# Optimization experiments

Measured on AMD Instinct MI355X. Metric: run time of the kernel, lower is better.

Reference implementation:

```python
import jax, jax.numpy as jnp
import numpy as np

B, S, D, H = 2, 2048, 1024, 16
DQ = D // H
EPS = 1e-5


def setup_inputs() -> dict:
    key = jax.random.key(0)
    ks = jax.random.split(key, 6)
    scale = 0.02
    return {
        "x": jax.random.normal(ks[0], (B, S, D), dtype=jnp.float32),
        "ln_g": jnp.ones((D,), dtype=jnp.float32),
        "ln_b": jnp.zeros((D,), dtype=jnp.float32),
        "Wq": jax.random.normal(ks[1], (D, D), dtype=jnp.float32) * scale,
        "bq": jnp.zeros((D,), dtype=jnp.float32),
        "Wk": jax.random.normal(ks[2], (D, D), dtype=jnp.float32) * scale,
        "bk": jnp.zeros((D,), dtype=jnp.float32),
        "Wv": jax.random.normal(ks[3], (D, D), dtype=jnp.float32) * scale,
        "bv": jnp.zeros((D,), dtype=jnp.float32),
        "Wo": jax.random.normal(ks[4], (D, D), dtype=jnp.float32) * scale,
        "bo": jnp.zeros((D,), dtype=jnp.float32),
    }


def reference(x, ln_g, ln_b, Wq, bq, Wk, bk, Wv, bv, Wo, bo):
    # pre-LayerNorm (torch default eps=1e-5, biased variance)
    mu = jnp.mean(x, axis=-1, keepdims=True)
    var = jnp.mean((x - mu) ** 2, axis=-1, keepdims=True)
    xn = (x - mu) * jax.lax.rsqrt(var + EPS) * ln_g + ln_b

    # QKV projections; weights stored [d_in, d_out]
    q = xn @ Wq + bq  # [B,S,D]
    k = xn @ Wk + bk
    v = xn @ Wv + bv

    # split heads -> [B,H,S,DQ]
    def heads(t):
        return t.reshape(B, S, H, DQ).transpose(0, 2, 1, 3)
    q, k, v = heads(q), heads(k), heads(v)

    scores = jnp.einsum("bhqd,bhkd->bhqk", q, k) / jnp.sqrt(jnp.float32(DQ))
    causal = jnp.tril(jnp.ones((S, S), dtype=bool))  # True = keep
    scores = jnp.where(causal, scores, -jnp.inf)
    probs = jax.nn.softmax(scores, axis=-1)
    attn = jnp.einsum("bhqk,bhkd->bhqd", probs, v)  # [B,H,S,DQ]

    # merge heads: [B,H,S,DQ] -> [B,S,H*DQ] (matches transpose/flatten/transpose)
    merged = attn.transpose(0, 2, 1, 3).reshape(B, S, D)
    out = merged @ Wo + bo
    return out + x
```

## Files before the change

### kernel.cpp

```cpp
#include <hip/hip_runtime.h>
#include <math.h>

#define BB 2
#define SS 2048
#define DD 1024
#define HH 16
#define DQK 64
#define NROWS (BB * SS)
#define NE ((size_t)BB * SS * DD)

using short8 = __attribute__((ext_vector_type(8))) short;
using f32x4  = __attribute__((ext_vector_type(4))) float;

__device__ __forceinline__ ushort f2bf(float f) {
  union { float f; unsigned u; } c; c.f = f;
  return (ushort)((c.u + 0x7fffu + ((c.u >> 16) & 1u)) >> 16);
}

__device__ __forceinline__ unsigned cvt_pk_bf16(float lo, float hi) {
  unsigned r;
  asm("v_cvt_pk_bf16_f32 %0, %1, %2" : "=v"(r) : "v"(lo), "v"(hi));
  return r;
}

__device__ __forceinline__ f32x4 mfma16(short8 a, short8 b, f32x4 c) {
  return __builtin_amdgcn_mfma_f32_16x16x32_bf16(a, b, c, 0, 0, 0);
}

__device__ __forceinline__ float fmax3(float a, float b, float c) {
  return fmaxf(fmaxf(a, b), c);
}

typedef __attribute__((address_space(1))) const unsigned gas_u32;
typedef __attribute__((address_space(3))) unsigned las_u32;
__device__ __forceinline__ void gload_lds16(const void* g, void* l) {
  __builtin_amdgcn_global_load_lds((gas_u32*)g, (las_u32*)l, 16, 0, 0);
}

__global__ __launch_bounds__(256) void prep(const float* __restrict__ x,
                                            const float* __restrict__ g,
                                            const float* __restrict__ bta,
                                            ushort* __restrict__ xn,
                                            const float* __restrict__ Wq,
                                            const float* __restrict__ Wk,
                                            const float* __restrict__ Wv,
                                            const float* __restrict__ Wo,
                                            ushort* __restrict__ wt) {
  const int t = threadIdx.x;
  if (blockIdx.x < NROWS / 4) {
    const int lane = t & 63, wid = t >> 6;
    const int row = blockIdx.x * 4 + wid;
    const float4* xr = (const float4*)(x + (size_t)row * DD);
    float4 v[4];
    float s = 0.f, ss = 0.f;
#pragma unroll
    for (int c = 0; c < 4; ++c) {
      v[c] = xr[c * 64 + lane];
      s  += (v[c].x + v[c].y) + (v[c].z + v[c].w);
      ss += (v[c].x * v[c].x + v[c].y * v[c].y) +
            (v[c].z * v[c].z + v[c].w * v[c].w);
    }
#pragma unroll
    for (int off = 32; off > 0; off >>= 1) {
      s  += __shfl_xor(s, off);
      ss += __shfl_xor(ss, off);
    }
    const float mu  = s * (1.0f / DD);
    const float var = ss * (1.0f / DD) - mu * mu;
    const float inv = rsqrtf(var + 1e-5f);
    ushort4* xo = (ushort4*)(xn + (size_t)row * DD);
#pragma unroll
    for (int c = 0; c < 4; ++c) {
      const float4 g4 = ((const float4*)g)[c * 64 + lane];
      const float4 b4 = ((const float4*)bta)[c * 64 + lane];
      ushort4 o;
      o.x = f2bf((v[c].x - mu) * inv * g4.x + b4.x);
      o.y = f2bf((v[c].y - mu) * inv * g4.y + b4.y);
      o.z = f2bf((v[c].z - mu) * inv * g4.z + b4.z);
      o.w = f2bf((v[c].w - mu) * inv * g4.w + b4.w);
      xo[c * 64 + lane] = o;
    }
  } else {
    __shared__ float tile[64][65];
    const int wb = blockIdx.x - NROWS / 4;
    const int z = wb >> 8;
    const int k0 = (wb & 15) * 64, n0 = ((wb >> 4) & 15) * 64;
    const float* W = (z == 0) ? Wq : (z == 1) ? Wk : (z == 2) ? Wv : Wo;
    ushort* dst = wt + (size_t)z * DD * DD;
    const int tr = t >> 4, tc = (t & 15) * 4;
#pragma unroll
    for (int rr = 0; rr < 64; rr += 16) {
      float4 v = *(const float4*)(W + (size_t)(k0 + rr + tr) * DD + n0 + tc);
      tile[rr + tr][tc + 0] = v.x;
      tile[rr + tr][tc + 1] = v.y;
      tile[rr + tr][tc + 2] = v.z;
      tile[rr + tr][tc + 3] = v.w;
    }
    __syncthreads();
#pragma unroll
    for (int rr = 0; rr < 64; rr += 16) {
      const int n = rr + tr;
      ushort4 o;
      o.x = f2bf(tile[tc + 0][n]);
      o.y = f2bf(tile[tc + 1][n]);
      o.z = f2bf(tile[tc + 2][n]);
      o.w = f2bf(tile[tc + 3][n]);
      *(ushort4*)(dst + (size_t)(n0 + n) * DD + k0 + tc) = o;
    }
  }
}

#define GEMM_CORE(Ag, Bg)                                                     \
  f32x4 acc[4][4];                                                            \
  _Pragma("unroll")                                                           \
  for (int m = 0; m < 4; ++m)                                                 \
    _Pragma("unroll")                                                         \
    for (int n = 0; n < 4; ++n) acc[m][n] = (f32x4){0.f, 0.f, 0.f, 0.f};     \
  const int cs = ((t & 3) * 16) ^ (((t >> 3) & 3) * 16);                      \
  const int fsw = ((r16 >> 1) & 3) * 16;                                      \
  {                                                                           \
    GSTAGE(Ag, Bg, 0, 0);                                                     \
    GSTAGE(Ag, Bg, 1, 32);                                                    \
    int cb = 0;                                                               \
    for (int k0 = 0; k0 < DD; k0 += 32) {                                     \
      __builtin_amdgcn_sched_barrier(0);                                      \
      if (k0 + 32 < DD) {                                                     \
        asm volatile("s_waitcnt vmcnt(4)" ::: "memory");                      \
      } else {                                                                \
        asm volatile("s_waitcnt vmcnt(0)" ::: "memory");                      \
      }                                                                       \
      __builtin_amdgcn_s_barrier();                                           \
      __builtin_amdgcn_sched_barrier(0);                                      \
      if (k0 + 64 < DD) {                                                     \
        int nb = cb + 2; if (nb >= 3) nb -= 3;                                \
        GSTAGE(Ag, Bg, nb, k0 + 64);                                          \
      }                                                                       \
      const char* Ac = (const char*)&As[cb][0][0];                            \
      const char* Bc = (const char*)&Bs[cb][0][0];                            \
      short8 af[4], bf[4];                                                    \
      _Pragma("unroll")                                                       \
      for (int m = 0; m < 4; ++m)                                             \
        af[m] = *(const short8*)(Ac + (wr * 64 + m * 16 + r16) * 64 +         \
                                 ((g * 16) ^ fsw));                           \
      _Pragma("unroll")                                                       \
      for (int n = 0; n < 4; ++n)                                             \
        bf[n] = *(const short8*)(Bc + (wc * 64 + n * 16 + r16) * 64 +         \
                                 ((g * 16) ^ fsw));                           \
      _Pragma("unroll")                                                       \
      for (int m = 0; m < 4; ++m)                                             \
        _Pragma("unroll")                                                     \
        for (int n = 0; n < 4; ++n) acc[m][n] = mfma16(af[m], bf[n], acc[m][n]); \
      cb = (cb + 1 == 3) ? 0 : cb + 1;                                        \
    }                                                                         \
  }

#define GSTAGE(Ag, Bg, buf, k0)                                               \
  {                                                                           \
    _Pragma("unroll")                                                         \
    for (int i = 0; i < 2; ++i) {                                             \
      gload_lds16(Ag + (size_t)(row0 + i * 64 + (t >> 2)) * (DD * 2) +        \
                      (k0) * 2 + cs,                                          \
                  (char*)&As[buf][0][0] + i * 4096 + t * 16);                 \
      gload_lds16(Bg + (size_t)(col0 + i * 64 + (t >> 2)) * (DD * 2) +        \
                      (k0) * 2 + cs,                                          \
                  (char*)&Bs[buf][0][0] + i * 4096 + t * 16);                 \
    }                                                                         \
  }

#define GEMM_CORE_O(Ag, Bg)                                                   \
  f32x4 acc[4][2];                                                            \
  _Pragma("unroll")                                                           \
  for (int m = 0; m < 4; ++m)                                                 \
    _Pragma("unroll")                                                         \
    for (int n = 0; n < 2; ++n) acc[m][n] = (f32x4){0.f, 0.f, 0.f, 0.f};     \
  const int cs = ((t & 3) * 16) ^ (((t >> 3) & 3) * 16);                      \
  const int fsw = ((r16 >> 1) & 3) * 16;                                      \
  {                                                                           \
    GSTAGE_O(Ag, Bg, 0, 0);                                                   \
    GSTAGE_O(Ag, Bg, 1, 32);                                                  \
    int cb = 0;                                                               \
    for (int k0 = 0; k0 < DD; k0 += 32) {                                     \
      __builtin_amdgcn_sched_barrier(0);                                      \
      if (k0 + 32 < DD) {                                                     \
        asm volatile("s_waitcnt vmcnt(3)" ::: "memory");                      \
      } else {                                                                \
        asm volatile("s_waitcnt vmcnt(0)" ::: "memory");                      \
      }                                                                       \
      __builtin_amdgcn_s_barrier();                                           \
      __builtin_amdgcn_sched_barrier(0);                                      \
      if (k0 + 64 < DD) {                                                     \
        int nb = cb + 2; if (nb >= 3) nb -= 3;                                \
        GSTAGE_O(Ag, Bg, nb, k0 + 64);                                        \
      }                                                                       \
      const char* Ac = (const char*)&As[cb][0][0];                            \
      const char* Bc = (const char*)&Bs[cb][0][0];                            \
      short8 af[4], bf[2];                                                    \
      _Pragma("unroll")                                                       \
      for (int m = 0; m < 4; ++m)                                             \
        af[m] = *(const short8*)(Ac + (wr * 64 + m * 16 + r16) * 64 +         \
                                 ((g * 16) ^ fsw));                           \
      _Pragma("unroll")                                                       \
      for (int n = 0; n < 2; ++n)                                             \
        bf[n] = *(const short8*)(Bc + (wc * 32 + n * 16 + r16) * 64 +         \
                                 ((g * 16) ^ fsw));                           \
      _Pragma("unroll")                                                       \
      for (int m = 0; m < 4; ++m)                                             \
        _Pragma("unroll")                                                     \
        for (int n = 0; n < 2; ++n) acc[m][n] = mfma16(af[m], bf[n], acc[m][n]); \
      cb = (cb + 1 == 3) ? 0 : cb + 1;                                        \
    }                                                                         \
  }

#define GSTAGE_O(Ag, Bg, buf, k0)                                             \
  {                                                                           \
    _Pragma("unroll")                                                         \
    for (int i = 0; i < 2; ++i)                                               \
      gload_lds16(Ag + (size_t)(row0 + i * 64 + (t >> 2)) * (DD * 2) +        \
                      (k0) * 2 + cs,                                          \
                  (char*)&As[buf][0][0] + i * 4096 + t * 16);                 \
    gload_lds16(Bg + (size_t)(col0 + (t >> 2)) * (DD * 2) + (k0) * 2 + cs,    \
                (char*)&Bs[buf][0][0] + t * 16);                              \
  }

__global__ __launch_bounds__(256, 3) void gemm_qkv(
    const ushort* __restrict__ A, const ushort* __restrict__ wt,
    const float* __restrict__ bq, const float* __restrict__ bk,
    const float* __restrict__ bv, ushort* __restrict__ qb,
    ushort* __restrict__ kb, ushort* __restrict__ vt) {
  __shared__ ushort As[3][128][32];
  __shared__ ushort Bs[3][128][32];
  const int t = threadIdx.x;
  const int lane = t & 63;
  const int w = t >> 6, wr = w >> 1, wc = w & 1;
  const int r16 = lane & 15, g = lane >> 4;
  const int row0 = blockIdx.x * 128;
  const int mat = blockIdx.y >> 3;
  const int col0 = (blockIdx.y & 7) * 128;
  const char* Ag = (const char*)A;
  const char* Bg = (const char*)(wt + (size_t)mat * DD * DD);
  const float* bias = (mat == 0) ? bq : (mat == 1) ? bk : bv;
  const float scl = (mat == 0) ? 0.125f * 1.44269504f : 1.0f;

  GEMM_CORE(Ag, Bg)

#pragma unroll
  for (int n = 0; n < 4; ++n) {
    const int c = col0 + wc * 64 + n * 16 + r16;
    const float bc = bias[c];
#pragma unroll
    for (int m = 0; m < 4; ++m) {
      const int rbase = row0 + wr * 64 + m * 16 + g * 4;
      if (mat < 2) {
        ushort* outb = (mat == 0) ? qb : kb;
#pragma unroll
        for (int e = 0; e < 4; ++e)
          outb[(size_t)(rbase + e) * DD + c] = f2bf((acc[m][n][e] + bc) * scl);
      } else {
        uint2 st;
        st.x = cvt_pk_bf16(acc[m][n][0] + bc, acc[m][n][1] + bc);
        st.y = cvt_pk_bf16(acc[m][n][2] + bc, acc[m][n][3] + bc);
        const size_t vrow = (size_t)((rbase >> 11) * HH + (c >> 6)) * DQK + (c & 63);
        *(uint2*)(vt + vrow * SS + (rbase & 2047)) = st;
      }
    }
  }
}

__global__ __launch_bounds__(256, 2) void gemm_o(
    const ushort* __restrict__ A, const ushort* __restrict__ Bt,
    const float* __restrict__ bias, const float* __restrict__ resid,
    float* __restrict__ outf) {
  __shared__ ushort As[3][128][32];
  __shared__ ushort Bs[3][64][32];
  const int t = threadIdx.x;
  const int lane = t & 63;
  const int w = t >> 6, wr = w >> 1, wc = w & 1;
  const int r16 = lane & 15, g = lane >> 4;
  const int row0 = blockIdx.x * 128;
  const int col0 = blockIdx.y * 64;
  const char* Ag = (const char*)A;
  const char* Bg = (const char*)Bt;

  GEMM_CORE_O(Ag, Bg)

#pragma unroll
  for (int n = 0; n < 2; ++n) {
    const int c = col0 + wc * 32 + n * 16 + r16;
    const float bc = bias[c];
#pragma unroll
    for (int m = 0; m < 4; ++m) {
      const int rbase = row0 + wr * 64 + m * 16 + g * 4;
#pragma unroll
      for (int e = 0; e < 4; ++e) {
        const size_t idx = (size_t)(rbase + e) * DD + c;
        outf[idx] = acc[m][n][e] + bc + resid[idx];
      }
    }
  }
}

__global__ __launch_bounds__(256, 4) void attn_mfma(const ushort* __restrict__ Q,
                                                    const ushort* __restrict__ K,
                                                    const ushort* __restrict__ Vt,
                                                    ushort* __restrict__ O) {
  __shared__ ushort Ks[2][64][64];
  __shared__ ushort Vs[2][64][64];

  const int t = threadIdx.x, lane = t & 63, ww = t >> 6;
  const int r16 = lane & 15, g = lane >> 4;

  const int bid = blockIdx.x;
  const int xcd = bid & 7;
  const int bh = xcd * 4 + ((bid >> 3) & 3);
  const int qb = 31 - (bid >> 5);
  const int b = bh >> 4, h = bh & 15;
  const size_t tokbase = (size_t)b * SS;
  const size_t hoff = (size_t)h * DQK;
  const int q0 = qb * 64 + ww * 16;
  const int nt = qb + 1;

  const int srow = t >> 3;
  const int scol = (t & 7) * 16;
  const int Cs = scol ^ (((srow & 3) | ((srow >> 1) & 4)) << 4);
  const char* Kb = (const char*)(K + tokbase * DD + hoff);
  const char* Vb = (const char*)(Vt + (size_t)bh * DQK * SS);
  const char* kbase0 = Kb + (size_t)srow * (DD * 2) + Cs;
  const char* kbase1 = Kb + (size_t)(srow + 32) * (DD * 2) + Cs;
  const char* vbase0 = Vb + (size_t)srow * (SS * 2) + Cs;
  const char* vbase1 = Vb + (size_t)(srow + 32) * (SS * 2) + Cs;
  char* ksd = (char*)&Ks[0][0][0] + ww * 1024;
  char* vsd = (char*)&Vs[0][0][0] + ww * 1024;

#define STAGE(BOFF, TILE)                                                     \
  {                                                                           \
    const size_t ko = (size_t)(TILE) << 17;                 \
    const size_t vo = (size_t)(TILE) << 7;                   \
    gload_lds16(kbase0 + ko, ksd + (BOFF));                                   \
    gload_lds16(kbase1 + ko, ksd + (BOFF) + 4096);                            \
    gload_lds16(vbase0 + vo, vsd + (BOFF));                                   \
    gload_lds16(vbase1 + vo, vsd + (BOFF) + 4096);                            \
  }

  const int sw = ((r16 & 3) | ((r16 >> 1) & 4)) << 4;
  const int rlo = (r16 & 3) + ((r16 >> 2) << 3);
  int offk[4][2], offv[4][2];
#pragma unroll
  for (int t2 = 0; t2 < 4; ++t2) {
    const int kk = rlo + (t2 & 1) * 4 + (t2 >> 1) * 32;
    const int sk = ((kk & 3) | ((kk >> 1) & 4)) << 4;
    offk[t2][0] = kk * 128 + ((g * 16) ^ sk);
    offk[t2][1] = kk * 128 + ((64 + g * 16) ^ sk);
  }
#pragma unroll
  for (int dt = 0; dt < 4; ++dt) {
    offv[dt][0] = (dt * 16 + r16) * 128 + ((g * 16) ^ sw);
    offv[dt][1] = (dt * 16 + r16) * 128 + ((64 + g * 16) ^ sw);
  }
  const char* KsB = (const char*)&Ks[0][0][0];
  const char* VsB = (const char*)&Vs[0][0][0];

  const short8 qc0 = *(const short8*)(Q + (tokbase + q0 + r16) * DD + hoff + g * 8);
  const short8 qc1 = *(const short8*)(Q + (tokbase + q0 + r16) * DD + hoff + 32 + g * 8);

  f32x4 o[4];
#pragma unroll
  for (int dt = 0; dt < 4; ++dt) o[dt] = (f32x4){0.f, 0.f, 0.f, 0.f};
  float rm = -INFINITY, rl = 0.f;

#define COMPUTE(BOFF, DOMASK, TLOC)                                           \
  {                                                                           \
    f32x4 s4[4];                                                              \
    __builtin_amdgcn_s_setprio(1);                                            \
    _Pragma("unroll")                                                         \
    for (int t2 = 0; t2 < 4; ++t2) {                                          \
      const short8 k0 = *(const short8*)(KsB + (BOFF) + offk[t2][0]);         \
      const short8 k1 = *(const short8*)(KsB + (BOFF) + offk[t2][1]);         \
      f32x4 s = mfma16(k0, qc0, (f32x4){0.f, 0.f, 0.f, 0.f});                 \
      s4[t2] = mfma16(k1, qc1, s);                                            \
    }                                                                         \
    __builtin_amdgcn_s_setprio(0);                                            \
    if (DOMASK) {                                                             \
      const int thrl = q0 + r16 - g * 8 - (TLOC) * 64;                        \
      _Pragma("unroll")                                                       \
      for (int t2 = 0; t2 < 4; ++t2) {                                        \
        const int bb = (t2 & 1) * 4 + (t2 >> 1) * 32;                         \
        _Pragma("unroll")                                                     \
        for (int r = 0; r < 4; ++r)                                           \
          s4[t2][r] = (bb + r <= thrl) ? s4[t2][r] : -INFINITY;               \
      }                                                                       \
    }                                                                         \
    float m0 = fmax3(s4[0][0], s4[0][1], s4[0][2]);                           \
    float m1 = fmax3(s4[0][3], s4[1][0], s4[1][1]);                           \
    float m2 = fmax3(s4[1][2], s4[1][3], s4[2][0]);                           \
    float m3 = fmax3(s4[2][1], s4[2][2], s4[2][3]);                           \
    float m4 = fmax3(s4[3][0], s4[3][1], s4[3][2]);                           \
    float mx = fmaxf(fmax3(m0, m1, m2), fmax3(m3, m4, s4[3][3]));             \
    if (!__all(mx - rm <= 8.f)) {                                             \
      float mf = fmaxf(mx, __shfl_xor(mx, 16));                               \
      mf = fmaxf(mf, __shfl_xor(mf, 32));                                     \
      const float mn = fmaxf(rm, mf);                                         \
      const float sc = __builtin_amdgcn_exp2f(rm - mn);                       \
      rl *= sc;                                                               \
      _Pragma("unroll")                                                       \
      for (int dt = 0; dt < 4; ++dt) o[dt] *= sc;                             \
      rm = mn;                                                                \
    }                                                                         \
    union { unsigned u[4]; short8 s; } pbu[2];                                \
    _Pragma("unroll")                                                         \
    for (int t2 = 0; t2 < 4; ++t2) {                                          \
      const float p0 = __builtin_amdgcn_exp2f(s4[t2][0] - rm);                \
      const float p1 = __builtin_amdgcn_exp2f(s4[t2][1] - rm);                \
      const float p2 = __builtin_amdgcn_exp2f(s4[t2][2] - rm);                \
      const float p3 = __builtin_amdgcn_exp2f(s4[t2][3] - rm);                \
      rl += (p0 + p1) + (p2 + p3);                                            \
      pbu[t2 >> 1].u[(t2 & 1) * 2 + 0] = cvt_pk_bf16(p0, p1);                 \
      pbu[t2 >> 1].u[(t2 & 1) * 2 + 1] = cvt_pk_bf16(p2, p3);                 \
    }                                                                         \
    __builtin_amdgcn_s_setprio(1);                                            \
    _Pragma("unroll")                                                         \
    for (int kc = 0; kc < 2; ++kc)                                            \
      _Pragma("unroll")                                                       \
      for (int dt = 0; dt < 4; ++dt) {                                        \
        const short8 vf = *(const short8*)(VsB + (BOFF) + offv[dt][kc]);      \
        o[dt] = mfma16(vf, pbu[kc].s, o[dt]);                                 \
      }                                                                       \
    __builtin_amdgcn_s_setprio(0);                                            \
  }

#define WAITBAR                                                               \
  __builtin_amdgcn_sched_barrier(0);                                          \
  asm volatile("s_waitcnt vmcnt(0)" ::: "memory");                            \
  __builtin_amdgcn_s_barrier();                                               \
  __builtin_amdgcn_sched_barrier(0);

  STAGE(0, 0);
  int tt = 0;
#pragma unroll 1
  for (; tt + 2 <= nt; tt += 2) {
    WAITBAR;
    STAGE(8192, tt + 1);
    COMPUTE(0, false, 0);
    WAITBAR;
    {
      int pj = tt + 2; if (pj >= nt) pj = 0;
      STAGE(0, pj);
    }
    COMPUTE(8192, (tt + 2 == nt), (tt + 1));
  }
  if (tt < nt) {
    WAITBAR;
    COMPUTE(0, true, tt);
  }
#undef STAGE
#undef COMPUTE
#undef WAITBAR

  rl += __shfl_xor(rl, 16);
  rl += __shfl_xor(rl, 32);
  const float inv = 1.0f / rl;
#pragma unroll
  for (int dt = 0; dt < 4; ++dt) {
    uint2 st;
    st.x = cvt_pk_bf16(o[dt][0] * inv, o[dt][1] * inv);
    st.y = cvt_pk_bf16(o[dt][2] * inv, o[dt][3] * inv);
    *(uint2*)(O + (tokbase + q0 + r16) * DD + hoff + dt * 16 + g * 4) = st;
  }
}

extern "C" void kernel_launch(void* const* d_in, const int* in_sizes, int n_in,
                              void* d_out, int out_size, void* d_ws, size_t ws_size,
                              hipStream_t stream) {
  const float* x    = (const float*)d_in[0];
  const float* ln_g = (const float*)d_in[1];
  const float* ln_b = (const float*)d_in[2];
  const float* Wq   = (const float*)d_in[3];
  const float* bq   = (const float*)d_in[4];
  const float* Wk   = (const float*)d_in[5];
  const float* bk   = (const float*)d_in[6];
  const float* Wv   = (const float*)d_in[7];
  const float* bv   = (const float*)d_in[8];
  const float* Wo   = (const float*)d_in[9];
  const float* bo   = (const float*)d_in[10];
  float* out = (float*)d_out;

  ushort* ws  = (ushort*)d_ws;
  ushort* xn  = ws;
  ushort* qb  = xn + NE;
  ushort* kb  = qb + NE;
  ushort* vt  = kb + NE;
  ushort* ab  = vt + NE;
  ushort* wt  = ab + NE;
  ushort* wot = wt + (size_t)3 * DD * DD;

  prep<<<NROWS / 4 + 1024, 256, 0, stream>>>(x, ln_g, ln_b, xn, Wq, Wk, Wv, Wo, wt);

  gemm_qkv<<<dim3(NROWS / 128, 24), 256, 0, stream>>>(xn, wt, bq, bk, bv,
                                                      qb, kb, vt);

  attn_mfma<<<BB * HH * (SS / 64), 256, 0, stream>>>(qb, kb, vt, ab);

  gemm_o<<<dim3(NROWS / 128, DD / 64), 256, 0, stream>>>(ab, wot, bo, x, out);
}
```

Baseline: 100.8 us.

## Replace QKV GEMM with 256x256-tile 8-wave kernel using quadrant-staged pipelining

Rewrites the QKV projection GEMM to use 256x256 output tiles per 512-thread block with K=64 steps, double-buffered LDS split into four half-tile quadrants. Each quadrant's next-stage load is issued just before computing the current quadrant, with setprio around the MFMA bursts. The aim is more data reuse per loaded byte and better overlap of global-to-LDS traffic with MFMA work. The cost is far fewer blocks (192 versus 768), a 128 KB LDS footprint, and heavier register pressure from 32 accumulators per thread, which can lower occupancy and leave the GPU underfilled.

```diff
diff --git a/kernel.cpp b/kernel.cpp
--- a/kernel.cpp
+++ b/kernel.cpp
@@ -110,62 +110,144 @@
   }
 }
 
-#define GEMM_CORE(Ag, Bg)                                                     \
-  f32x4 acc[4][4];                                                            \
-  _Pragma("unroll")                                                           \
-  for (int m = 0; m < 4; ++m)                                                 \
-    _Pragma("unroll")                                                         \
-    for (int n = 0; n < 4; ++n) acc[m][n] = (f32x4){0.f, 0.f, 0.f, 0.f};     \
-  const int cs = ((t & 3) * 16) ^ (((t >> 3) & 3) * 16);                      \
-  const int fsw = ((r16 >> 1) & 3) * 16;                                      \
+#define QWAIT4                                                                \
+  __builtin_amdgcn_sched_barrier(0);                                          \
+  asm volatile("s_waitcnt vmcnt(4)" ::: "memory");                            \
+  __builtin_amdgcn_s_barrier();                                               \
+  __builtin_amdgcn_sched_barrier(0);
+
+#define QWAIT0                                                                \
+  __builtin_amdgcn_sched_barrier(0);                                          \
+  asm volatile("s_waitcnt vmcnt(0)" ::: "memory");                            \
+  __builtin_amdgcn_s_barrier();                                               \
+  __builtin_amdgcn_sched_barrier(0);
+
+#define QBAR                                                                  \
+  __builtin_amdgcn_sched_barrier(0);                                          \
+  __builtin_amdgcn_s_barrier();                                               \
+  __builtin_amdgcn_sched_barrier(0);
+
+#define QSTAGE(LN, ab, h, ptr, kt)                                            \
   {                                                                           \
-    GSTAGE(Ag, Bg, 0, 0);                                                     \
-    GSTAGE(Ag, Bg, 1, 32);                                                    \
-    int cb = 0;                                                               \
-    for (int k0 = 0; k0 < DD; k0 += 32) {                                     \
-      __builtin_amdgcn_sched_barrier(0);                                      \
-      if (k0 + 32 < DD) {                                                     \
-        asm volatile("s_waitcnt vmcnt(4)" ::: "memory");                      \
-      } else {                                                                \
-        asm volatile("s_waitcnt vmcnt(0)" ::: "memory");                      \
-      }                                                                       \
-      __builtin_amdgcn_s_barrier();                                           \
-      __builtin_amdgcn_sched_barrier(0);                                      \
-      if (k0 + 64 < DD) {                                                     \
-        int nb = cb + 2; if (nb >= 3) nb -= 3;                                \
-        GSTAGE(Ag, Bg, nb, k0 + 64);                                          \
-      }                                                                       \
-      const char* Ac = (const char*)&As[cb][0][0];                            \
-      const char* Bc = (const char*)&Bs[cb][0][0];                            \
-      short8 af[4], bf[4];                                                    \
-      _Pragma("unroll")                                                       \
-      for (int m = 0; m < 4; ++m)                                             \
-        af[m] = *(const short8*)(Ac + (wr * 64 + m * 16 + r16) * 64 +         \
-                                 ((g * 16) ^ fsw));                           \
-      _Pragma("unroll")                                                       \
-      for (int n = 0; n < 4; ++n)                                             \
-        bf[n] = *(const short8*)(Bc + (wc * 64 + n * 16 + r16) * 64 +         \
-                                 ((g * 16) ^ fsw));                           \
-      _Pragma("unroll")                                                       \
-      for (int m = 0; m < 4; ++m)                                             \
+    const char* s_ = (ptr) + (size_t)(kt) * 128;                              \
+    char* d_ = (LN) + ((ab) * 2 + (h)) * 16384 + dst0;                        \
+    gload_lds16(s_, d_);                                                      \
+    gload_lds16(s_ + (size_t)(64 * DD * 2), d_ + 8192);                       \
+  }
+
+#define DOQUAD(LC, mh, nh)                                                    \
+  {                                                                           \
+    const char* Ah_ = (LC) + (mh) * 16384;                                    \
+    const char* Bh_ = (LC) + (2 + (nh)) * 16384;                              \
+    short8 a_[4][2], b_[2][2];                                                \
+    _Pragma("unroll")                                                         \
+    for (int i = 0; i < 4; ++i) {                                             \
+      a_[i][0] = *(const short8*)(Ah_ + aoff[i] + swzk0);                     \
+      a_[i][1] = *(const short8*)(Ah_ + aoff[i] + swzk1);                     \
+    }                                                                         \
+    _Pragma("unroll")                                                         \
+    for (int j = 0; j < 2; ++j) {                                             \
+      b_[j][0] = *(const short8*)(Bh_ + boff[j] + swzk0);                     \
+      b_[j][1] = *(const short8*)(Bh_ + boff[j] + swzk1);                     \
+    }                                                                         \
+    __builtin_amdgcn_s_setprio(1);                                            \
+    _Pragma("unroll")                                                         \
+    for (int kf = 0; kf < 2; ++kf)                                            \
+      _Pragma("unroll")                                                       \
+      for (int i = 0; i < 4; ++i)                                             \
         _Pragma("unroll")                                                     \
-        for (int n = 0; n < 4; ++n) acc[m][n] = mfma16(af[m], bf[n], acc[m][n]); \
-      cb = (cb + 1 == 3) ? 0 : cb + 1;                                        \
-    }                                                                         \
-  }
-
-#define GSTAGE(Ag, Bg, buf, k0)                                               \
-  {                                                                           \
-    _Pragma("unroll")                                                         \
-    for (int i = 0; i < 2; ++i) {                                             \
-      gload_lds16(Ag + (size_t)(row0 + i * 64 + (t >> 2)) * (DD * 2) +        \
-                      (k0) * 2 + cs,                                          \
-                  (char*)&As[buf][0][0] + i * 4096 + t * 16);                 \
-      gload_lds16(Bg + (size_t)(col0 + i * 64 + (t >> 2)) * (DD * 2) +        \
-                      (k0) * 2 + cs,                                          \
-                  (char*)&Bs[buf][0][0] + i * 4096 + t * 16);                 \
-    }                                                                         \
-  }
+        for (int j = 0; j < 2; ++j)                                           \
+          acc[(mh) * 4 + i][(nh) * 2 + j] =                                   \
+              mfma16(a_[i][kf], b_[j][kf], acc[(mh) * 4 + i][(nh) * 2 + j]);  \
+    __builtin_amdgcn_s_setprio(0);                                            \
+  }
+
+__global__ __launch_bounds__(512, 2) void gemm_qkv8(
+    const ushort* __restrict__ A, const ushort* __restrict__ wt,
+    const float* __restrict__ bq, const float* __restrict__ bk,
+    const float* __restrict__ bv, ushort* __restrict__ qb,
+    ushort* __restrict__ kb, ushort* __restrict__ vt) {
+  __shared__ ushort lds[2 * 2 * 2 * 128 * 64];
+  const int t = threadIdx.x;
+  const int w = t >> 6, lane = t & 63;
+  const int wr = w >> 2, wc = w & 3;
+  const int r16 = lane & 15, g = lane >> 4;
+  const int row0 = blockIdx.x * 256;
+  const int mat = blockIdx.y >> 2;
+  const int col0 = (blockIdx.y & 3) * 256;
+  const char* Ag = (const char*)A;
+  const char* Bg = (const char*)(wt + (size_t)mat * DD * DD);
+  const float* bias = (mat == 0) ? bq : (mat == 1) ? bk : bv;
+  const float scl = (mat == 0) ? 0.125f * 1.44269504f : 1.0f;
+
+  const int rst = t >> 3;
+  const int swz = (t & 7) ^ (rst & 7);
+  const char* pA0 = Ag + (size_t)(row0 + rst) * (DD * 2) + swz * 16;
+  const char* pA1 = pA0 + (size_t)128 * (DD * 2);
+  const char* pB0 = Bg + (size_t)(col0 + rst) * (DD * 2) + swz * 16;
+  const char* pB1 = pB0 + (size_t)128 * (DD * 2);
+  char* Lb = (char*)&lds[0];
+  const int dst0 = w * 1024;
+
+  const int swzk0 = (g ^ (r16 & 7)) * 16;
+  const int swzk1 = ((4 + g) ^ (r16 & 7)) * 16;
+  int aoff[4], boff[2];
+#pragma unroll
+  for (int i = 0; i < 4; ++i) aoff[i] = (wr * 64 + i * 16 + r16) * 128;
+#pragma unroll
+  for (int j = 0; j < 2; ++j) boff[j] = (wc * 32 + j * 16 + r16) * 128;
+
+  f32x4 acc[8][4];
+#pragma unroll
+  for (int m = 0; m < 8; ++m)
+#pragma unroll
+    for (int n = 0; n < 4; ++n) acc[m][n] = (f32x4){0.f, 0.f, 0.f, 0.f};
+
+  QSTAGE(Lb, 0, 0, pA0, 0);
+  QSTAGE(Lb, 1, 0, pB0, 0);
+  QSTAGE(Lb, 0, 1, pA1, 0);
+  QSTAGE(Lb, 1, 1, pB1, 0);
+
+#pragma unroll 1
+  for (int kt = 0; kt < 16; ++kt) {
+    const char* Lc = Lb + (kt & 1) * 65536;
+    char* Ln = Lb + ((kt + 1) & 1) * 65536;
+    const int kn = kt + 1;
+    if (kn < 16) {
+      QWAIT4; QSTAGE(Ln, 0, 0, pA0, kn); DOQUAD(Lc, 0, 0);
+      QWAIT4; QSTAGE(Ln, 1, 0, pB0, kn); DOQUAD(Lc, 1, 0);
+      QWAIT4; QSTAGE(Ln, 0, 1, pA1, kn); DOQUAD(Lc, 0, 1);
+      QWAIT4; QSTAGE(Ln, 1, 1, pB1, kn); DOQUAD(Lc, 1, 1);
+    } else {
+      QWAIT0; DOQUAD(Lc, 0, 0);
+      QBAR;   DOQUAD(Lc, 1, 0);
+      QBAR;   DOQUAD(Lc, 0, 1);
+      QBAR;   DOQUAD(Lc, 1, 1);
+    }
+  }
+
+#pragma unroll
+  for (int n = 0; n < 4; ++n) {
+    const int c = col0 + (n >> 1) * 128 + wc * 32 + (n & 1) * 16 + r16;
+    const float bc = bias[c];
+#pragma unroll
+    for (int m = 0; m < 8; ++m) {
+      const int rbase = row0 + (m >> 2) * 128 + wr * 64 + (m & 3) * 16 + g * 4;
+      if (mat < 2) {
+        ushort* outb = (mat == 0) ? qb : kb;
+#pragma unroll
+        for (int e = 0; e < 4; ++e)
+          outb[(size_t)(rbase + e) * DD + c] = f2bf((acc[m][n][e] + bc) * scl);
+      } else {
+        uint2 st;
+        st.x = cvt_pk_bf16(acc[m][n][0] + bc, acc[m][n][1] + bc);
+        st.y = cvt_pk_bf16(acc[m][n][2] + bc, acc[m][n][3] + bc);
+        const size_t vrow = (size_t)((rbase >> 11) * HH + (c >> 6)) * DQK + (c & 63);
+        *(uint2*)(vt + vrow * SS + (rbase & 2047)) = st;
+      }
+    }
+  }
+}
 
 #define GEMM_CORE_O(Ag, Bg)                                                   \
   f32x4 acc[4][2];                                                            \
@@ -222,50 +304,6 @@
                 (char*)&Bs[buf][0][0] + t * 16);                              \
   }
 
-__global__ __launch_bounds__(256, 3) void gemm_qkv(
-    const ushort* __restrict__ A, const ushort* __restrict__ wt,
-    const float* __restrict__ bq, const float* __restrict__ bk,
-    const float* __restrict__ bv, ushort* __restrict__ qb,
-    ushort* __restrict__ kb, ushort* __restrict__ vt) {
-  __shared__ ushort As[3][128][32];
-  __shared__ ushort Bs[3][128][32];
-  const int t = threadIdx.x;
-  const int lane = t & 63;
-  const int w = t >> 6, wr = w >> 1, wc = w & 1;
-  const int r16 = lane & 15, g = lane >> 4;
-  const int row0 = blockIdx.x * 128;
-  const int mat = blockIdx.y >> 3;
-  const int col0 = (blockIdx.y & 7) * 128;
-  const char* Ag = (const char*)A;
-  const char* Bg = (const char*)(wt + (size_t)mat * DD * DD);
-  const float* bias = (mat == 0) ? bq : (mat == 1) ? bk : bv;
-  const float scl = (mat == 0) ? 0.125f * 1.44269504f : 1.0f;
-
-  GEMM_CORE(Ag, Bg)
-
-#pragma unroll
-  for (int n = 0; n < 4; ++n) {
-    const int c = col0 + wc * 64 + n * 16 + r16;
-    const float bc = bias[c];
-#pragma unroll
-    for (int m = 0; m < 4; ++m) {
-      const int rbase = row0 + wr * 64 + m * 16 + g * 4;
-      if (mat < 2) {
-        ushort* outb = (mat == 0) ? qb : kb;
-#pragma unroll
-        for (int e = 0; e < 4; ++e)
-          outb[(size_t)(rbase + e) * DD + c] = f2bf((acc[m][n][e] + bc) * scl);
-      } else {
-        uint2 st;
-        st.x = cvt_pk_bf16(acc[m][n][0] + bc, acc[m][n][1] + bc);
-        st.y = cvt_pk_bf16(acc[m][n][2] + bc, acc[m][n][3] + bc);
-        const size_t vrow = (size_t)((rbase >> 11) * HH + (c >> 6)) * DQK + (c & 63);
-        *(uint2*)(vt + vrow * SS + (rbase & 2047)) = st;
-      }
-    }
-  }
-}
-
 __global__ __launch_bounds__(256, 2) void gemm_o(
     const ushort* __restrict__ A, const ushort* __restrict__ Bt,
     const float* __restrict__ bias, const float* __restrict__ resid,
@@ -494,8 +532,8 @@
 
   prep<<<NROWS / 4 + 1024, 256, 0, stream>>>(x, ln_g, ln_b, xn, Wq, Wk, Wv, Wo, wt);
 
-  gemm_qkv<<<dim3(NROWS / 128, 24), 256, 0, stream>>>(xn, wt, bq, bk, bv,
-                                                      qb, kb, vt);
+  gemm_qkv8<<<dim3(NROWS / 256, 12), 512, 0, stream>>>(xn, wt, bq, bk, bv,
+                                                       qb, kb, vt);
 
   attn_mfma<<<BB * HH * (SS / 64), 256, 0, stream>>>(qb, kb, vt, ab);
 
```

Result: slower. 181.5 us (+80.0%).
